# Kernel optimization log

Hardware: AMD Instinct MI355X
Metric: run time of the kernel (lower is better)

Reference implementation:

```python
import jax, jax.numpy as jnp
import numpy as np
from jax import lax

B, A, SEQ, FIN = 512, 16, 50, 6
H, H2, T, G, S = 256, 128, 60, 64, 6
GR0, GR1 = -50.0, 50.0
CELL = (GR1 - GR0) / G
NTYPES, EMB = 10, 16
NENC, NL = 5, 2

def setup_inputs() -> dict:
    key = jax.random.key(0)
    ks = jax.random.split(key, 40)
    def rn(k, shape, scale=0.05):
        return (jax.random.normal(k, shape) * scale).astype(jnp.float32)
    history = jax.random.normal(ks[0], (B, A, SEQ, FIN), dtype=jnp.float32)
    types = jax.random.randint(ks[1], (B,), 0, NTYPES)
    history = history.at[:, 0, 0, 5].set(types.astype(jnp.float32))
    d = dict(history=history)
    d['emb'] = rn(ks[2], (NTYPES, EMB))
    d['fe_W1'] = rn(ks[3], (FIN + EMB, H)); d['fe_b1'] = jnp.zeros((H,), jnp.float32)
    d['fe_W2'] = rn(ks[4], (H, H));        d['fe_b2'] = jnp.zeros((H,), jnp.float32)
    d['enc_Wih'] = rn(ks[5], (NENC, NL, H, 3 * H))
    d['enc_Whh'] = rn(ks[6], (NENC, NL, H, 3 * H))
    d['enc_bih'] = rn(ks[7], (NENC, NL, 3 * H))
    d['enc_bhh'] = rn(ks[8], (NENC, NL, 3 * H))
    d['dec_Wih0'] = rn(ks[9], (2, 3 * H)); d['dec_Whh0'] = rn(ks[10], (H, 3 * H))
    d['dec_bih0'] = rn(ks[11], (3 * H));   d['dec_bhh0'] = rn(ks[12], (3 * H))
    d['dec_Wih1'] = rn(ks[13], (H, 3 * H)); d['dec_Whh1'] = rn(ks[14], (H, 3 * H))
    d['dec_bih1'] = rn(ks[15], (3 * H));    d['dec_bhh1'] = rn(ks[16], (3 * H))
    d['hg_W1'] = rn(ks[17], (H, H));   d['hg_b1'] = jnp.zeros((H,), jnp.float32)
    d['hg_W2'] = rn(ks[18], (H, H2));  d['hg_b2'] = jnp.zeros((H2,), jnp.float32)
    d['hg_W3'] = rn(ks[19], (H2, T * 2)); d['hg_b3'] = jnp.zeros((T * 2,), jnp.float32)
    d['ce_W1'] = rn(ks[20], (H, H2));  d['ce_b1'] = jnp.zeros((H2,), jnp.float32)
    d['ce_W2'] = rn(ks[21], (H2, T));  d['ce_b2'] = jnp.zeros((T,), jnp.float32)
    d['hp_W1'] = rn(ks[22], (H, H));   d['hp_b1'] = jnp.zeros((H,), jnp.float32)
    d['hp_W2'] = rn(ks[23], (H, G * G)); d['hp_b2'] = jnp.zeros((G * G,), jnp.float32)
    return d

def _gru_cell(xt, h, Wih, Whh, bih, bhh):
    # torch GRU gate order: r, z, n
    gi = xt @ Wih + bih
    gh = h @ Whh + bhh
    Hd = h.shape[-1]
    r = jax.nn.sigmoid(gi[:, :Hd] + gh[:, :Hd])
    z = jax.nn.sigmoid(gi[:, Hd:2 * Hd] + gh[:, Hd:2 * Hd])
    n = jnp.tanh(gi[:, 2 * Hd:] + r * gh[:, 2 * Hd:])
    return (1.0 - z) * n + z * h

def _forward(history, emb, fe_W1, fe_b1, fe_W2, fe_b2,
             enc_Wih, enc_Whh, enc_bih, enc_bhh,
             dec_Wih0, dec_Whh0, dec_bih0, dec_bhh0,
             dec_Wih1, dec_Whh1, dec_bih1, dec_bhh1,
             hg_W1, hg_b1, hg_W2, hg_b2, hg_W3, hg_b3,
             ce_W1, ce_b1, ce_W2, ce_b2, hp_W1, hp_b1, hp_W2, hp_b2):
    ego = history[:, 0]                                   # [B,SEQ,6]
    etype = jnp.clip(ego[:, 0, 5].astype(jnp.int32), 0, 9)
    # type -> encoder index (vehicle,pedestrian,cyclist,bus,default)
    eidx = jnp.array([0, 1, 4, 2, 3, 4, 4, 4, 4, 4], jnp.int32)[etype]
    te = emb[etype]                                       # [B,16]
    x_in = jnp.concatenate([ego, jnp.broadcast_to(te[:, None, :], (B, SEQ, EMB))], axis=-1)
    feat = jax.nn.relu(x_in @ fe_W1 + fe_b1) @ fe_W2 + fe_b2  # [B,SEQ,H]

    # 2-layer GRU with per-example (type-gathered) weights
    x_cur = feat.transpose(1, 0, 2)                       # [SEQ,B,H]
    h_finals = []
    for l in range(NL):
        Wih = enc_Wih[eidx, l]; Whh = enc_Whh[eidx, l]    # [B,H,3H]
        bih = enc_bih[eidx, l]; bhh = enc_bhh[eidx, l]    # [B,3H]
        def step(h, xt, Wih=Wih, Whh=Whh, bih=bih, bhh=bhh):
            gi = jnp.einsum('bd,bdg->bg', xt, Wih) + bih
            gh = jnp.einsum('bh,bhg->bg', h, Whh) + bhh
            r = jax.nn.sigmoid(gi[:, :H] + gh[:, :H])
            z = jax.nn.sigmoid(gi[:, H:2 * H] + gh[:, H:2 * H])
            n = jnp.tanh(gi[:, 2 * H:] + r * gh[:, 2 * H:])
            hn = (1.0 - z) * n + z * h
            return hn, hn
        h_last, ys = lax.scan(step, jnp.zeros((B, H), feat.dtype), x_cur)
        x_cur = ys
        h_finals.append(h_last)
    enc_h0, enc_h1 = h_finals

    # decoder GRU, single timestep: x = last ego position
    x0 = ego[:, -1, :2]
    h0 = _gru_cell(x0, enc_h0, dec_Wih0, dec_Whh0, dec_bih0, dec_bhh0)
    h1 = _gru_cell(h0, enc_h1, dec_Wih1, dec_Whh1, dec_bih1, dec_bhh1)
    last_hidden = h1                                      # [B,H]

    traj = (jax.nn.relu(jax.nn.relu(last_hidden @ hg_W1 + hg_b1) @ hg_W2 + hg_b2) @ hg_W3 + hg_b3)
    traj = traj.reshape(B, T, 2)
    conf = jax.nn.relu(last_hidden @ ce_W1 + ce_b1) @ ce_W2 + ce_b2   # [B,T]

    key = jax.random.key(42)
    k_noise, k_samp = jax.random.split(key)
    noise = jax.random.normal(k_noise, (T, B, H), last_hidden.dtype)
    scale = (0.1 * jnp.arange(T, dtype=last_hidden.dtype) / T)[:, None, None]
    th = last_hidden[None] + noise * scale                # [T,B,H]
    logits = jax.nn.relu(th @ hp_W1 + hp_b1) @ hp_W2 + hp_b2  # [T,B,G*G]

    # vectorized multinomial over (samples, timesteps, batch)
    idx = jax.random.categorical(k_samp, logits, shape=(S - 1, T, B))  # int [S-1,T,B]
    x_idx = (idx % G).astype(jnp.float32)
    y_idx = (idx // G).astype(jnp.float32)
    pts = jnp.stack([GR0 + x_idx * CELL + CELL / 2,
                     GR0 + y_idx * CELL + CELL / 2], axis=-1)  # [S-1,T,B,2]
    pts = pts.transpose(2, 0, 1, 3)                       # [B,S-1,T,2]

    predictions = jnp.concatenate([traj[:, None], pts], axis=1)  # [B,S,T,2]
    decay = jnp.float32(0.9) ** jnp.arange(S, dtype=jnp.float32)
    confidences = conf.mean(axis=1)[:, None] * decay[None, :]    # [B,S]
    return predictions, confidences

def reference(history, emb, fe_W1, fe_b1, fe_W2, fe_b2,
              enc_Wih, enc_Whh, enc_bih, enc_bhh,
              dec_Wih0, dec_Whh0, dec_bih0, dec_bhh0,
              dec_Wih1, dec_Whh1, dec_bih1, dec_bhh1,
              hg_W1, hg_b1, hg_W2, hg_b2, hg_W3, hg_b3,
              ce_W1, ce_b1, ce_W2, ce_b2, hp_W1, hp_b1, hp_W2, hp_b2):
    return _forward(history, emb, fe_W1, fe_b1, fe_W2, fe_b2,
                    enc_Wih, enc_Whh, enc_bih, enc_bhh,
                    dec_Wih0, dec_Whh0, dec_bih0, dec_bhh0,
                    dec_Wih1, dec_Whh1, dec_bih1, dec_bhh1,
                    hg_W1, hg_b1, hg_W2, hg_b2, hg_W3, hg_b3,
                    ce_W1, ce_b1, ce_W2, ce_b2, hp_W1, hp_b1, hp_W2, hp_b2)
```

## Files before the change

kernel.cpp:

```cpp
#include <hip/hip_runtime.h>
#include <stdint.h>
#include <math.h>

#define JAX_PARTITIONABLE 1

#define B_ 512
#define SEQ_ 50
#define H_ 256
#define H2_ 128
#define T_ 60
#define S_ 6
#define EMB_ 16
#define NL_ 2
#define TG_ 768
#define CAT_ 4096
#define GUMBEL_N 629145600u
#define NOISE_N 7864320u

typedef float f32x2 __attribute__((ext_vector_type(2)));

#define PKFMA_LO(acc, w, h) \
  asm("v_pk_fma_f32 %0, %1, %2, %0 op_sel:[0,0,0] op_sel_hi:[1,0,1]" : "+v"(acc) : "v"(w), "v"(h))
#define PKFMA_HI(acc, w, h) \
  asm("v_pk_fma_f32 %0, %1, %2, %0 op_sel:[0,1,0] op_sel_hi:[1,1,1]" : "+v"(acc) : "v"(w), "v"(h))

__host__ __device__ inline uint32_t rotl32(uint32_t x, int r) {
#if defined(__HIP_DEVICE_COMPILE__)
  return __builtin_amdgcn_alignbit(x, x, 32 - r);
#else
  return (x << r) | (x >> (32 - r));
#endif
}

__host__ __device__ inline void tf2x32(uint32_t k0, uint32_t k1, uint32_t x0, uint32_t x1,
                                       uint32_t& o0, uint32_t& o1) {
  uint32_t ks2 = k0 ^ k1 ^ 0x1BD11BDAu;
  x0 += k0; x1 += k1;
#define TFR(r) do { x0 += x1; x1 = rotl32(x1, r); x1 ^= x0; } while (0)
  TFR(13); TFR(15); TFR(26); TFR(6);
  x0 += k1; x1 += ks2 + 1u;
  TFR(17); TFR(29); TFR(16); TFR(24);
  x0 += ks2; x1 += k0 + 2u;
  TFR(13); TFR(15); TFR(26); TFR(6);
  x0 += k0; x1 += k1 + 3u;
  TFR(17); TFR(29); TFR(16); TFR(24);
  x0 += k1; x1 += ks2 + 4u;
  TFR(13); TFR(15); TFR(26); TFR(6);
  x0 += ks2; x1 += k0 + 5u;
#undef TFR
  o0 = x0; o1 = x1;
}

__device__ inline uint32_t jax_bits(uint32_t k0, uint32_t k1, uint32_t i, uint32_t n) {
#if JAX_PARTITIONABLE
  (void)n;
  uint32_t a, b;
  tf2x32(k0, k1, 0u, i, a, b);
  return a ^ b;
#else
  uint32_t half = n >> 1;
  uint32_t lo = (i < half) ? i : (i - half);
  uint32_t a, b;
  tf2x32(k0, k1, lo, lo + half, a, b);
  return (i < half) ? a : b;
#endif
}

__device__ inline float bits_to_f01(uint32_t bits) {
  return __uint_as_float((bits >> 9) | 0x3f800000u) - 1.0f;
}

__device__ inline float erfinv_f(float x) {
  double xd = (double)x;
  float w = (float)(-log((1.0 - xd) * (1.0 + xd)));
  float p;
  if (w < 5.0f) {
    w = __fadd_rn(w, -2.5f);
    p = 2.81022636e-08f;
    p = __fadd_rn(3.43273939e-07f, __fmul_rn(p, w));
    p = __fadd_rn(-3.5233877e-06f, __fmul_rn(p, w));
    p = __fadd_rn(-4.39150654e-06f, __fmul_rn(p, w));
    p = __fadd_rn(0.00021858087f, __fmul_rn(p, w));
    p = __fadd_rn(-0.00125372503f, __fmul_rn(p, w));
    p = __fadd_rn(-0.00417768164f, __fmul_rn(p, w));
    p = __fadd_rn(0.246640727f, __fmul_rn(p, w));
    p = __fadd_rn(1.50140941f, __fmul_rn(p, w));
  } else {
    w = __fadd_rn(__fsqrt_rn(w), -3.0f);
    p = -0.000200214257f;
    p = __fadd_rn(0.000100950558f, __fmul_rn(p, w));
    p = __fadd_rn(0.00134934322f, __fmul_rn(p, w));
    p = __fadd_rn(-0.00367342844f, __fmul_rn(p, w));
    p = __fadd_rn(0.00573950773f, __fmul_rn(p, w));
    p = __fadd_rn(-0.0076224613f, __fmul_rn(p, w));
    p = __fadd_rn(0.00943887047f, __fmul_rn(p, w));
    p = __fadd_rn(1.00167406f, __fmul_rn(p, w));
    p = __fadd_rn(2.83297682f, __fmul_rn(p, w));
  }
  return __fmul_rn(p, x);
}

__device__ inline float gumbel_f32(uint32_t bits) {
  float f = bits_to_f01(bits);
  float u = fmaxf(f, 1.17549435e-38f);
  float l1 = logf(u);
  return -logf(-l1);
}

__device__ inline uint32_t orderkey(float s) {
  uint32_t sb = __float_as_uint(s);
  return (sb & 0x80000000u) ? ~sb : (sb | 0x80000000u);
}

__global__ __launch_bounds__(512) void k_init(const float* __restrict__ hist,
                                              float* __restrict__ x0buf, int* __restrict__ ip) {
  int b = threadIdx.x;
  if (b < B_) {
    float tv = hist[b * 4800 + 5];
    int et = (int)tv;
    et = et < 0 ? 0 : (et > 9 ? 9 : et);
    const int mp[10] = {0, 1, 4, 2, 3, 4, 4, 4, 4, 4};
    ip[b] = et;
    ip[512 + b] = mp[et];
    x0buf[b * 2 + 0] = hist[b * 4800 + 49 * 6 + 0];
    x0buf[b * 2 + 1] = hist[b * 4800 + 49 * 6 + 1];
  }
  __syncthreads();
  if (b == 0) {
    int cnt[5] = {0, 0, 0, 0, 0};
    for (int i = 0; i < B_; i++) cnt[ip[512 + i]]++;
    int off[6];
    off[0] = 0;
    for (int e = 0; e < 5; e++) off[e + 1] = off[e] + cnt[e];
    int pos[5];
    for (int e = 0; e < 5; e++) pos[e] = off[e];
    for (int i = 0; i < B_; i++) { int e = ip[512 + i]; ip[1024 + pos[e]++] = i; }
    int* tbl = ip + 1536;
    int nrt = 0;
    for (int e = 0; e < 5; e++) {
      int n = cnt[e];
      for (int s = 0; s < n; s += 16) {
        tbl[1 + nrt] = e;
        tbl[37 + nrt] = off[e] + s;
        tbl[73 + nrt] = (n - s) < 16 ? (n - s) : 16;
        nrt++;
      }
    }
    tbl[0] = nrt;
  }
}

__global__ void k_zero(uint32_t* p, int n) {
  int i = blockIdx.x * blockDim.x + threadIdx.x;
  if (i < n) p[i] = 0u;
}

__global__ __launch_bounds__(256) void k_pack(const float* __restrict__ Wih,
                                              const float* __restrict__ Whh,
                                              float4* __restrict__ wp) {
  int i = blockIdx.x * 256 + threadIdx.x;
  if (i >= 20 * 65536) return;
  int cl = i & 31;
  int k  = (i >> 5) & 255;
  int cg = (i >> 13) & 7;
  int em = i >> 16;
  int m = em & 1;
  int el = em >> 1;
  int c = cg * 32 + cl;
  const float* W = (m ? Whh : Wih) + (size_t)el * H_ * TG_;
  float4 v;
  v.x = W[k * TG_ + c];
  v.y = W[k * TG_ + H_ + c];
  v.z = W[k * TG_ + 2 * H_ + c];
  v.w = 0.0f;
  wp[i] = v;
}

__global__ __launch_bounds__(256) void k_feat(const float* __restrict__ hist, const float* __restrict__ emb,
    const float* __restrict__ W1, const float* __restrict__ b1,
    const float* __restrict__ W2, const float* __restrict__ b2,
    const int* __restrict__ ip, float* __restrict__ featbuf) {
  __shared__ float xs[16][22];
  __shared__ float t1[16][H_];
  int row0 = blockIdx.x * 16;
  int tid = threadIdx.x;
  for (int idx = tid; idx < 16 * 22; idx += 256) {
    int r = idx / 22, c = idx % 22;
    int g = row0 + r;
    int b = g / SEQ_, s = g % SEQ_;
    xs[r][c] = (c < 6) ? hist[b * 4800 + s * 6 + c] : emb[ip[b] * EMB_ + (c - 6)];
  }
  __syncthreads();
  int j = tid;
  {
    double acc[16];
    for (int r = 0; r < 16; r++) acc[r] = 0.0;
    for (int k = 0; k < 22; k++) {
      double w = (double)W1[k * H_ + j];
      for (int r = 0; r < 16; r++) acc[r] += (double)xs[r][k] * w;
    }
    double bb = (double)b1[j];
    for (int r = 0; r < 16; r++) t1[r][j] = fmaxf((float)(acc[r] + bb), 0.0f);
  }
  __syncthreads();
  {
    double acc[16];
    for (int r = 0; r < 16; r++) acc[r] = 0.0;
    for (int k = 0; k < H_; k++) {
      double w = (double)W2[k * H_ + j];
      for (int r = 0; r < 16; r++) acc[r] += (double)t1[r][k] * w;
    }
    double bb = (double)b2[j];
    for (int r = 0; r < 16; r++) {
      float v = (float)(acc[r] + bb);
      int g = row0 + r;
      int b = g / SEQ_, s = g % SEQ_;
      featbuf[(size_t)s * (B_ * H_) + (size_t)b * H_ + j] = v;
    }
  }
}

__device__ __forceinline__ void gi_block_p(float (*xs)[H_], int* rowb,
    int rt, int cg, int tid,
    const float* __restrict__ x, float* __restrict__ gi_out,
    const float4* __restrict__ wpack, const float* __restrict__ bih_base,
    int layer, const int* __restrict__ ip) {
  const int* tbl = ip + 1536;
  const int* order = ip + 1024;
  int nrt = tbl[0];
  if (rt >= nrt) return;
  int e = tbl[1 + rt];
  int start = tbl[37 + rt];
  int nr = tbl[73 + rt];
  for (int idx = tid; idx < 16 * H_; idx += 256) {
    int r = idx >> 8, k = idx & 255;
    int rr = (r < nr) ? r : 0;
    int b = order[start + rr];
    if (k == 0) rowb[r] = b;
    xs[r][k] = x[b * H_ + k];
  }
  __syncthreads();
  int j = tid & 31, rs = tid >> 5;
  int c = cg * 32 + j;
  int el = e * NL_ + layer;
  const float4* wp = wpack + (((size_t)(el * 2 + 0) * 8 + cg) * 256) * 32 + j;
  const float* bih = bih_base + (size_t)el * TG_;
  double ar0 = 0, ar1 = 0, az0 = 0, az1 = 0, an0 = 0, an1 = 0;
  for (int k = 0; k < H_; k += 4) {
    float4 w0 = wp[(k + 0) * 32], w1 = wp[(k + 1) * 32];
    float4 w2 = wp[(k + 2) * 32], w3 = wp[(k + 3) * 32];
    float4 xa = *(const float4*)&xs[rs][k];
    float4 xb = *(const float4*)&xs[rs + 8][k];
    ar0 += (double)xa.x * (double)w0.x; ar1 += (double)xb.x * (double)w0.x;
    az0 += (double)xa.x * (double)w0.y; az1 += (double)xb.x * (double)w0.y;
    an0 += (double)xa.x * (double)w0.z; an1 += (double)xb.x * (double)w0.z;
    ar0 += (double)xa.y * (double)w1.x; ar1 += (double)xb.y * (double)w1.x;
    az0 += (double)xa.y * (double)w1.y; az1 += (double)xb.y * (double)w1.y;
    an0 += (double)xa.y * (double)w1.z; an1 += (double)xb.y * (double)w1.z;
    ar0 += (double)xa.z * (double)w2.x; ar1 += (double)xb.z * (double)w2.x;
    az0 += (double)xa.z * (double)w2.y; az1 += (double)xb.z * (double)w2.y;
    an0 += (double)xa.z * (double)w2.z; an1 += (double)xb.z * (double)w2.z;
    ar0 += (double)xa.w * (double)w3.x; ar1 += (double)xb.w * (double)w3.x;
    az0 += (double)xa.w * (double)w3.y; az1 += (double)xb.w * (double)w3.y;
    an0 += (double)xa.w * (double)w3.z; an1 += (double)xb.w * (double)w3.z;
  }
  int cr = c, cz = H_ + c, cn = 2 * H_ + c;
  double br = (double)bih[cr], bz = (double)bih[cz], bn = (double)bih[cn];
  for (int p = 0; p < 2; p++) {
    int r = rs + 8 * p;
    if (r >= nr) continue;
    int b = rowb[r];
    gi_out[b * TG_ + cr] = (float)((p ? ar1 : ar0) + br);
    gi_out[b * TG_ + cz] = (float)((p ? az1 : az0) + bz);
    gi_out[b * TG_ + cn] = (float)((p ? an1 : an0) + bn);
  }
}

__device__ __forceinline__ void step_block_p(float (*hs)[H_], int* rowb,
    int rt, int cg, int tid,
    const float* __restrict__ gi_in, const float* __restrict__ hin,
    float* __restrict__ hout, float* __restrict__ ys,
    const float4* __restrict__ wpack, const float* __restrict__ bhh_base,
    int layer, const int* __restrict__ ip) {
  const int* tbl = ip + 1536;
  const int* order = ip + 1024;
  int nrt = tbl[0];
  if (rt >= nrt) return;
  int e = tbl[1 + rt];
  int start = tbl[37 + rt];
  int nr = tbl[73 + rt];
  for (int idx = tid; idx < 16 * H_; idx += 256) {
    int r = idx >> 8, k = idx & 255;
    int rr = (r < nr) ? r : 0;
    int b = order[start + rr];
    if (k == 0) rowb[r] = b;
    hs[r][k] = hin[b * H_ + k];
  }
  __syncthreads();
  int j = tid & 31, rs = tid >> 5;
  int c = cg * 32 + j;
  int el = e * NL_ + layer;
  const float4* wp = wpack + (((size_t)(el * 2 + 1) * 8 + cg) * 256) * 32 + j;
  const float* bhh = bhh_base + (size_t)el * TG_;
  double gr0 = 0, gr1 = 0, gz0 = 0, gz1 = 0, gn0 = 0, gn1 = 0;
  for (int k = 0; k < H_; k += 4) {
    float4 w0 = wp[(k + 0) * 32], w1 = wp[(k + 1) * 32];
    float4 w2 = wp[(k + 2) * 32], w3 = wp[(k + 3) * 32];
    float4 ha = *(const float4*)&hs[rs][k];
    float4 hb = *(const float4*)&hs[rs + 8][k];
    gr0 += (double)ha.x * (double)w0.x; gr1 += (double)hb.x * (double)w0.x;
    gz0 += (double)ha.x * (double)w0.y; gz1 += (double)hb.x * (double)w0.y;
    gn0 += (double)ha.x * (double)w0.z; gn1 += (double)hb.x * (double)w0.z;
    gr0 += (double)ha.y * (double)w1.x; gr1 += (double)hb.y * (double)w1.x;
    gz0 += (double)ha.y * (double)w1.y; gz1 += (double)hb.y * (double)w1.y;
    gn0 += (double)ha.y * (double)w1.z; gn1 += (double)hb.y * (double)w1.z;
    gr0 += (double)ha.z * (double)w2.x; gr1 += (double)hb.z * (double)w2.x;
    gz0 += (double)ha.z * (double)w2.y; gz1 += (double)hb.z * (double)w2.y;
    gn0 += (double)ha.z * (double)w2.z; gn1 += (double)hb.z * (double)w2.z;
    gr0 += (double)ha.w * (double)w3.x; gr1 += (double)hb.w * (double)w3.x;
    gz0 += (double)ha.w * (double)w3.y; gz1 += (double)hb.w * (double)w3.y;
    gn0 += (double)ha.w * (double)w3.z; gn1 += (double)hb.w * (double)w3.z;
  }
  int cr = c, cz = H_ + c, cn = 2 * H_ + c;
  double bhr = (double)bhh[cr], bhz = (double)bhh[cz], bhn = (double)bhh[cn];
  for (int p = 0; p < 2; p++) {
    int r = rs + 8 * p;
    if (r >= nr) continue;
    int b = rowb[r];
    double gir = (double)gi_in[b * TG_ + cr];
    double giz = (double)gi_in[b * TG_ + cz];
    double gin = (double)gi_in[b * TG_ + cn];
    double ghr = (p ? gr1 : gr0) + bhr;
    double ghz = (p ? gz1 : gz0) + bhz;
    double ghn = (p ? gn1 : gn0) + bhn;
    double rr = 1.0 / (1.0 + exp(-(gir + ghr)));
    double zz = 1.0 / (1.0 + exp(-(giz + ghz)));
    double nn = tanh(gin + rr * ghn);
    double hv = (double)hs[r][c];
    float hnew = (float)((1.0 - zz) * nn + zz * hv);
    hout[b * H_ + c] = hnew;
    if (ys) ys[b * H_ + c] = hnew;
  }
}

__device__ __forceinline__ void gi_block_u(float (*xs)[H_], int* rowb,
    int rt, int cg, int tid,
    const float* __restrict__ x, float* __restrict__ gi_out,
    const float* __restrict__ Wih_base, const float* __restrict__ bih_base,
    int layer, const int* __restrict__ ip) {
  const int* tbl = ip + 1536;
  const int* order = ip + 1024;
  int nrt = tbl[0];
  if (rt >= nrt) return;
  int e = tbl[1 + rt];
  int start = tbl[37 + rt];
  int nr = tbl[73 + rt];
  for (int idx = tid; idx < 16 * H_; idx += 256) {
    int r = idx >> 8, k = idx & 255;
    int rr = (r < nr) ? r : 0;
    int b = order[start + rr];
    if (k == 0) rowb[r] = b;
    xs[r][k] = x[b * H_ + k];
  }
  __syncthreads();
  size_t woff = (size_t)(e * NL_ + layer);
  const float* Wih = Wih_base + woff * (size_t)H_ * TG_;
  const float* bih = bih_base + woff * TG_;
  int j = tid & 31, rs = tid >> 5;
  int c = cg * 32 + j;
  int cr = c, cz = H_ + c, cn = 2 * H_ + c;
  double ar0 = 0, ar1 = 0, az0 = 0, az1 = 0, an0 = 0, an1 = 0;
  for (int k = 0; k < H_; k++) {
    float wr = Wih[k * TG_ + cr], wz = Wih[k * TG_ + cz], wn = Wih[k * TG_ + cn];
    float x0 = xs[rs][k], x1 = xs[rs + 8][k];
    ar0 += (double)x0 * wr; ar1 += (double)x1 * wr;
    az0 += (double)x0 * wz; az1 += (double)x1 * wz;
    an0 += (double)x0 * wn; an1 += (double)x1 * wn;
  }
  double br = (double)bih[cr], bz = (double)bih[cz], bn = (double)bih[cn];
  for (int p = 0; p < 2; p++) {
    int r = rs + 8 * p;
    if (r >= nr) continue;
    int b = rowb[r];
    gi_out[b * TG_ + cr] = (float)((p ? ar1 : ar0) + br);
    gi_out[b * TG_ + cz] = (float)((p ? az1 : az0) + bz);
    gi_out[b * TG_ + cn] = (float)((p ? an1 : an0) + bn);
  }
}

__device__ __forceinline__ void step_block_u(float (*hs)[H_], int* rowb,
    int rt, int cg, int tid,
    const float* __restrict__ gi_in, const float* __restrict__ hin,
    float* __restrict__ hout, float* __restrict__ ys,
    const float* __restrict__ Whh_base, const float* __restrict__ bhh_base,
    int layer, const int* __restrict__ ip) {
  const int* tbl = ip + 1536;
  const int* order = ip + 1024;
  int nrt = tbl[0];
  if (rt >= nrt) return;
  int e = tbl[1 + rt];
  int start = tbl[37 + rt];
  int nr = tbl[73 + rt];
  for (int idx = tid; idx < 16 * H_; idx += 256) {
    int r = idx >> 8, k = idx & 255;
    int rr = (r < nr) ? r : 0;
    int b = order[start + rr];
    if (k == 0) rowb[r] = b;
    hs[r][k] = hin[b * H_ + k];
  }
  __syncthreads();
  size_t woff = (size_t)(e * NL_ + layer);
  const float* Whh = Whh_base + woff * (size_t)H_ * TG_;
  const float* bhh = bhh_base + woff * TG_;
  int j = tid & 31, rs = tid >> 5;
  int c = cg * 32 + j;
  int cr = c, cz = H_ + c, cn = 2 * H_ + c;
  double gr0 = 0, gr1 = 0, gz0 = 0, gz1 = 0, gn0 = 0, gn1 = 0;
  for (int k = 0; k < H_; k++) {
    float wr = Whh[k * TG_ + cr], wz = Whh[k * TG_ + cz], wn = Whh[k * TG_ + cn];
    float h0 = hs[rs][k], h1 = hs[rs + 8][k];
    gr0 += (double)h0 * wr; gr1 += (double)h1 * wr;
    gz0 += (double)h0 * wz; gz1 += (double)h1 * wz;
    gn0 += (double)h0 * wn; gn1 += (double)h1 * wn;
  }
  double bhr = (double)bhh[cr], bhz = (double)bhh[cz], bhn = (double)bhh[cn];
  for (int p = 0; p < 2; p++) {
    int r = rs + 8 * p;
    if (r >= nr) continue;
    int b = rowb[r];
    double gir = (double)gi_in[b * TG_ + cr];
    double giz = (double)gi_in[b * TG_ + cz];
    double gin = (double)gi_in[b * TG_ + cn];
    double ghr = (p ? gr1 : gr0) + bhr;
    double ghz = (p ? gz1 : gz0) + bhz;
    double ghn = (p ? gn1 : gn0) + bhn;
    double rr = 1.0 / (1.0 + exp(-(gir + ghr)));
    double zz = 1.0 / (1.0 + exp(-(giz + ghz)));
    double nn = tanh(gin + rr * ghn);
    double hv = (double)hs[r][c];
    float hnew = (float)((1.0 - zz) * nn + zz * hv);
    hout[b * H_ + c] = hnew;
    if (ys) ys[b * H_ + c] = hnew;
  }
}

template <bool PACKED>
__global__ __launch_bounds__(256) void k_pipe(int d,
    const float* __restrict__ feat, float* __restrict__ ys0,
    float* __restrict__ gi0, float* __restrict__ gi1,
    float* __restrict__ h0A, float* __restrict__ h0B,
    float* __restrict__ h1A, float* __restrict__ h1B,
    const float* __restrict__ Wih, const float* __restrict__ Whh,
    const float* __restrict__ bih, const float* __restrict__ bhh,
    const float4* __restrict__ wpack, const int* __restrict__ ip) {
  __shared__ float sb[16][H_];
  __shared__ int rowb[16];
  int g = blockIdx.x;
  int grp = g / 288, bx = g % 288;
  int rt = bx >> 3, cg = bx & 7;
  int tid = threadIdx.x;
  if (grp == 0) {
    int t = d; if (t >= SEQ_) return;
    if (PACKED) gi_block_p(sb, rowb, rt, cg, tid, feat + (size_t)t * 131072,
                           gi0 + (size_t)(t & 1) * 393216, wpack, bih, 0, ip);
    else        gi_block_u(sb, rowb, rt, cg, tid, feat + (size_t)t * 131072,
                           gi0 + (size_t)(t & 1) * 393216, Wih, bih, 0, ip);
  } else if (grp == 1) {
    int t = d - 1; if (t < 0 || t >= SEQ_) return;
    const float* hin = (t & 1) ? h0B : h0A;
    float* hout = (t & 1) ? h0A : h0B;
    if (PACKED) step_block_p(sb, rowb, rt, cg, tid, gi0 + (size_t)(t & 1) * 393216,
                             hin, hout, ys0 + (size_t)t * 131072, wpack, bhh, 0, ip);
    else        step_block_u(sb, rowb, rt, cg, tid, gi0 + (size_t)(t & 1) * 393216,
                             hin, hout, ys0 + (size_t)t * 131072, Whh, bhh, 0, ip);
  } else if (grp == 2) {
    int t = d - 2; if (t < 0 || t >= SEQ_) return;
    if (PACKED) gi_block_p(sb, rowb, rt, cg, tid, ys0 + (size_t)t * 131072,
                           gi1 + (size_t)(t & 1) * 393216, wpack, bih, 1, ip);
    else        gi_block_u(sb, rowb, rt, cg, tid, ys0 + (size_t)t * 131072,
                           gi1 + (size_t)(t & 1) * 393216, Wih, bih, 1, ip);
  } else {
    int t = d - 3; if (t < 0 || t >= SEQ_) return;
    const float* hin = (t & 1) ? h1B : h1A;
    float* hout = (t & 1) ? h1A : h1B;
    if (PACKED) step_block_p(sb, rowb, rt, cg, tid, gi1 + (size_t)(t & 1) * 393216,
                             hin, hout, nullptr, wpack, bhh, 1, ip);
    else        step_block_u(sb, rowb, rt, cg, tid, gi1 + (size_t)(t & 1) * 393216,
                             hin, hout, nullptr, Whh, bhh, 1, ip);
  }
}

template <int D1>
__global__ __launch_bounds__(256) void k_gru(
    const float* __restrict__ x, const float* __restrict__ hin,
    float* __restrict__ hout,
    const float* __restrict__ Wih, const float* __restrict__ Whh,
    const float* __restrict__ bih, const float* __restrict__ bhh) {
  __shared__ float xs[16][(D1 == 2) ? 2 : H_];
  __shared__ float hs[16][H_];
  int bx = blockIdx.x, by = blockIdx.y;
  int start = bx * 16;
  int tid = threadIdx.x;
  for (int idx = tid; idx < 16 * H_; idx += 256) {
    int r = idx >> 8, k = idx & 255;
    int b = start + r;
    hs[r][k] = hin[b * H_ + k];
    if (D1 == H_) xs[r][k] = x[b * H_ + k];
    else if (k < D1) xs[r][k] = x[b * D1 + k];
  }
  __syncthreads();
  int j = tid & 31, rs = tid >> 5;
  int hc = by * 32 + j;
  int cr = hc, cz = H_ + hc, cn = 2 * H_ + hc;
  double ra0 = 0, ra1 = 0, za0 = 0, za1 = 0, ni0 = 0, ni1 = 0, nh0 = 0, nh1 = 0;
  for (int k = 0; k < H_; k++) {
    float wrh = Whh[k * TG_ + cr], wzh = Whh[k * TG_ + cz], wnh = Whh[k * TG_ + cn];
    float h0v = hs[rs][k], h1v = hs[rs + 8][k];
    ra0 += (double)h0v * wrh; ra1 += (double)h1v * wrh;
    za0 += (double)h0v * wzh; za1 += (double)h1v * wzh;
    nh0 += (double)h0v * wnh; nh1 += (double)h1v * wnh;
    if (D1 == H_) {
      float wri = Wih[k * TG_ + cr], wzi = Wih[k * TG_ + cz], wni = Wih[k * TG_ + cn];
      float x0v = xs[rs][k], x1v = xs[rs + 8][k];
      ra0 += (double)x0v * wri; ra1 += (double)x1v * wri;
      za0 += (double)x0v * wzi; za1 += (double)x1v * wzi;
      ni0 += (double)x0v * wni; ni1 += (double)x1v * wni;
    }
  }
  if (D1 != H_) {
    for (int k = 0; k < D1; k++) {
      float wri = Wih[k * TG_ + cr], wzi = Wih[k * TG_ + cz], wni = Wih[k * TG_ + cn];
      float x0v = xs[rs][k], x1v = xs[rs + 8][k];
      ra0 += (double)x0v * wri; ra1 += (double)x1v * wri;
      za0 += (double)x0v * wzi; za1 += (double)x1v * wzi;
      ni0 += (double)x0v * wni; ni1 += (double)x1v * wni;
    }
  }
  double br_i = (double)bih[cr], bz_i = (double)bih[cz], bn_i = (double)bih[cn];
  double br_h = (double)bhh[cr], bz_h = (double)bhh[cz], bn_h = (double)bhh[cn];
  for (int p = 0; p < 2; p++) {
    int r = rs + 8 * p;
    double ra = p ? ra1 : ra0, za = p ? za1 : za0, ni = p ? ni1 : ni0, nh = p ? nh1 : nh0;
    double rr = 1.0 / (1.0 + exp(-(ra + br_i + br_h)));
    double zz = 1.0 / (1.0 + exp(-(za + bz_i + bz_h)));
    double nn = tanh((ni + bn_i) + rr * (nh + bn_h));
    double hv = (double)hs[r][hc];
    float hnew = (float)((1.0 - zz) * nn + zz * hv);
    hout[(start + r) * H_ + hc] = hnew;
  }
}

__global__ __launch_bounds__(256) void k_heads(const float* __restrict__ lh,
    const float* __restrict__ hgW1, const float* __restrict__ hgb1,
    const float* __restrict__ hgW2, const float* __restrict__ hgb2,
    const float* __restrict__ hgW3, const float* __restrict__ hgb3,
    const float* __restrict__ ceW1, const float* __restrict__ ceb1,
    const float* __restrict__ ceW2, const float* __restrict__ ceb2,
    float* __restrict__ out) {
  __shared__ float hsm[16][H_];
  __shared__ float t1[16][H_];
  __shared__ float t2[16][H2_];
  __shared__ float c2s[16][T_];
  int row0 = blockIdx.x * 16;
  int tid = threadIdx.x;
  for (int idx = tid; idx < 16 * H_; idx += 256) {
    int r = idx >> 8, k = idx & 255;
    hsm[r][k] = lh[(size_t)(row0 + r) * H_ + k];
  }
  __syncthreads();
  {
    int j = tid;
    for (int r = 0; r < 16; r++) {
      double a = 0;
      for (int k = 0; k < H_; k++) a += (double)hsm[r][k] * (double)hgW1[k * H_ + j];
      t1[r][j] = fmaxf((float)(a + (double)hgb1[j]), 0.0f);
    }
  }
  __syncthreads();
  if (tid < H2_) {
    int j = tid;
    for (int r = 0; r < 16; r++) {
      double a = 0;
      for (int k = 0; k < H_; k++) a += (double)t1[r][k] * (double)hgW2[k * H2_ + j];
      t2[r][j] = fmaxf((float)(a + (double)hgb2[j]), 0.0f);
    }
  }
  __syncthreads();
  if (tid < 2 * T_) {
    int j = tid;
    for (int r = 0; r < 16; r++) {
      double a = 0;
      for (int k = 0; k < H2_; k++) a += (double)t2[r][k] * (double)hgW3[k * (2 * T_) + j];
      float v = (float)(a + (double)hgb3[j]);
      int b = row0 + r;
      int t = j >> 1, c = j & 1;
      out[(((size_t)b * S_ + 0) * T_ + t) * 2 + c] = v;
    }
  }
  __syncthreads();
  if (tid < H2_) {
    int j = tid;
    for (int r = 0; r < 16; r++) {
      double a = 0;
      for (int k = 0; k < H_; k++) a += (double)hsm[r][k] * (double)ceW1[k * H2_ + j];
      t2[r][j] = fmaxf((float)(a + (double)ceb1[j]), 0.0f);
    }
  }
  __syncthreads();
  if (tid < T_) {
    int j = tid;
    for (int r = 0; r < 16; r++) {
      double a = 0;
      for (int k = 0; k < H2_; k++) a += (double)t2[r][k] * (double)ceW2[k * T_ + j];
      c2s[r][j] = (float)(a + (double)ceb2[j]);
    }
  }
  __syncthreads();
  if (tid < 16) {
    int r = tid;
    int b = row0 + r;
    double s = 0;
    for (int j = 0; j < T_; j++) s += (double)c2s[r][j];
    float m = (float)(s / 60.0);
    for (int sd = 0; sd < S_; sd++) {
      float d = (float)pow((double)0.9f, (double)sd);
      out[368640 + b * S_ + sd] = __fmul_rn(m, d);
    }
  }
}

__global__ __launch_bounds__(256) void k_hp1(const float* __restrict__ lh,
    const float* __restrict__ W1, const float* __restrict__ b1,
    float* __restrict__ h1buf, uint32_t nk0, uint32_t nk1) {
  __shared__ float th[16][H_];
  int row0 = blockIdx.x * 16;
  int tid = threadIdx.x;
  const float SQRT2F = 1.4142135623730951f;
  const float LO = -0x1.fffffep-1f;
  for (int idx = tid; idx < 16 * H_; idx += 256) {
    int r = idx >> 8, k = idx & 255;
    int g = row0 + r;
    int t = g / B_, b = g % B_;
    uint32_t i = ((uint32_t)t * B_ + (uint32_t)b) * H_ + (uint32_t)k;
    uint32_t bits = jax_bits(nk0, nk1, i, NOISE_N);
    float f = bits_to_f01(bits);
    float u = fmaxf(LO, __fadd_rn(__fmul_rn(f, 2.0f), LO));
    float nz = __fmul_rn(SQRT2F, erfinv_f(u));
    float sc = __fdiv_rn(__fmul_rn(0.1f, (float)t), 60.0f);
    th[r][k] = __fadd_rn(lh[(size_t)b * H_ + k], __fmul_rn(nz, sc));
  }
  __syncthreads();
  int j = tid;
  double acc[16];
  for (int r = 0; r < 16; r++) acc[r] = 0.0;
  for (int k = 0; k < H_; k++) {
    double w = (double)W1[k * H_ + j];
    for (int r = 0; r < 16; r++) acc[r] += (double)th[r][k] * w;
  }
  double bb = (double)b1[j];
  for (int r = 0; r < 16; r++)
    h1buf[(size_t)(row0 + r) * H_ + j] = fmaxf((float)(acc[r] + bb), 0.0f);
}

__global__ __launch_bounds__(256) void k_hp2(const float* __restrict__ h1buf,
    const float* __restrict__ W2, const float* __restrict__ b2,
    unsigned long long* __restrict__ samples, uint32_t sk0, uint32_t sk1) {
  __shared__ float h1[16][H_];
  int row0 = blockIdx.x * 16;
  int cat0 = blockIdx.y * 256;
  int tid = threadIdx.x;
  for (int idx = tid; idx < 16 * H_ / 4; idx += 256) {
    int r = idx >> 6, k4 = (idx & 63) << 2;
    *(float4*)&h1[r][k4] = *(const float4*)&h1buf[(size_t)(row0 + r) * H_ + k4];
  }
  __syncthreads();
  int wave = tid >> 6;
  int lane = tid & 63;
  int catA = cat0 + 4 * lane;
  int rbase = 4 * wave;

  f32x2 acc[4][2];
#pragma unroll
  for (int r = 0; r < 4; r++) { acc[r][0] = (f32x2)0.0f; acc[r][1] = (f32x2)0.0f; }
  const float* w2p = W2 + catA;
  for (int k = 0; k < H_; k += 4) {
    float4 hv[4];
    hv[0] = *(const float4*)&h1[rbase + 0][k];
    hv[1] = *(const float4*)&h1[rbase + 1][k];
    hv[2] = *(const float4*)&h1[rbase + 2][k];
    hv[3] = *(const float4*)&h1[rbase + 3][k];
    float4 wv[4];
#pragma unroll
    for (int kk = 0; kk < 4; kk++) wv[kk] = *(const float4*)&w2p[(size_t)(k + kk) * CAT_];
#pragma unroll
    for (int kk = 0; kk < 4; kk++) {
      f32x2 wlo; wlo.x = wv[kk].x; wlo.y = wv[kk].y;
      f32x2 whi; whi.x = wv[kk].z; whi.y = wv[kk].w;
#pragma unroll
      for (int r = 0; r < 4; r++) {
        f32x2 hp;
        if (kk & 2) { hp.x = (&hv[r].x)[2]; hp.y = (&hv[r].x)[3]; }
        else        { hp.x = (&hv[r].x)[0]; hp.y = (&hv[r].x)[1]; }
        if (kk & 1) { PKFMA_HI(acc[r][0], wlo, hp); PKFMA_HI(acc[r][1], whi, hp); }
        else        { PKFMA_LO(acc[r][0], wlo, hp); PKFMA_LO(acc[r][1], whi, hp); }
      }
    }
  }
  float lg[4][4];
  float4 b4 = *(const float4*)&b2[catA];
#pragma unroll
  for (int r = 0; r < 4; r++) {
    lg[r][0] = __fadd_rn(acc[r][0].x, b4.x);
    lg[r][1] = __fadd_rn(acc[r][0].y, b4.y);
    lg[r][2] = __fadd_rn(acc[r][1].x, b4.z);
    lg[r][3] = __fadd_rn(acc[r][1].y, b4.w);
  }

  int t = row0 / B_;
  int bbase = row0 % B_;
#pragma unroll
  for (int s = 0; s < S_ - 1; s++) {
#pragma unroll
    for (int q = 0; q < 4; q++) {
      int brow = bbase + rbase + q;
      uint32_t ibase = (((uint32_t)s * T_ + (uint32_t)t) * B_ + (uint32_t)brow) * CAT_ + (uint32_t)catA;
      float sc0 = __fadd_rn(gumbel_f32(jax_bits(sk0, sk1, ibase + 0u, GUMBEL_N)), lg[q][0]);
      float sc1 = __fadd_rn(gumbel_f32(jax_bits(sk0, sk1, ibase + 1u, GUMBEL_N)), lg[q][1]);
      float sc2 = __fadd_rn(gumbel_f32(jax_bits(sk0, sk1, ibase + 2u, GUMBEL_N)), lg[q][2]);
      float sc3 = __fadd_rn(gumbel_f32(jax_bits(sk0, sk1, ibase + 3u, GUMBEL_N)), lg[q][3]);
      float bs = sc0; int bc = catA;
      if (sc1 > bs) { bs = sc1; bc = catA + 1; }
      if (sc2 > bs) { bs = sc2; bc = catA + 2; }
      if (sc3 > bs) { bs = sc3; bc = catA + 3; }
      float mv = bs;
      for (int off = 1; off < 64; off <<= 1)
        mv = fmaxf(mv, __shfl_xor(mv, off, 64));
      unsigned long long mask = __ballot(bs == mv);
      int src = __ffsll(mask) - 1;
      int wcat = __shfl(bc, src, 64);
      if (lane == 0) {
        unsigned long long p =
            (((unsigned long long)orderkey(mv)) << 32) | (unsigned long long)(~(uint32_t)wcat);
        atomicMax(&samples[((size_t)s * T_ + t) * B_ + brow], p);
      }
    }
  }
}

__global__ void k_emit(const unsigned long long* __restrict__ samples, float* __restrict__ out) {
  int gid = blockIdx.x * blockDim.x + threadIdx.x;
  if (gid >= (S_ - 1) * T_ * B_) return;
  int b = gid % B_;
  int t = (gid / B_) % T_;
  int s = gid / (B_ * T_);
  unsigned long long v = samples[gid];
  uint32_t cat = ~(uint32_t)(v & 0xFFFFFFFFu);
  float xi = (float)(cat & 63u);
  float yi = (float)(cat >> 6);
  float px = -50.0f + xi * 1.5625f + 0.78125f;
  float py = -50.0f + yi * 1.5625f + 0.78125f;
  size_t o = (((size_t)b * S_ + (size_t)(s + 1)) * T_ + t) * 2;
  out[o] = px;
  out[o + 1] = py;
}

extern "C" void kernel_launch(void* const* d_in, const int* in_sizes, int n_in,
                              void* d_out, int out_size, void* d_ws, size_t ws_size,
                              hipStream_t stream) {
  (void)in_sizes; (void)n_in; (void)out_size;
  const float* hist   = (const float*)d_in[0];
  const float* emb    = (const float*)d_in[1];
  const float* feW1   = (const float*)d_in[2];
  const float* feb1   = (const float*)d_in[3];
  const float* feW2   = (const float*)d_in[4];
  const float* feb2   = (const float*)d_in[5];
  const float* encWih = (const float*)d_in[6];
  const float* encWhh = (const float*)d_in[7];
  const float* encbih = (const float*)d_in[8];
  const float* encbhh = (const float*)d_in[9];
  const float* dWih0  = (const float*)d_in[10];
  const float* dWhh0  = (const float*)d_in[11];
  const float* dbih0  = (const float*)d_in[12];
  const float* dbhh0  = (const float*)d_in[13];
  const float* dWih1  = (const float*)d_in[14];
  const float* dWhh1  = (const float*)d_in[15];
  const float* dbih1  = (const float*)d_in[16];
  const float* dbhh1  = (const float*)d_in[17];
  const float* hgW1   = (const float*)d_in[18];
  const float* hgb1   = (const float*)d_in[19];
  const float* hgW2   = (const float*)d_in[20];
  const float* hgb2   = (const float*)d_in[21];
  const float* hgW3   = (const float*)d_in[22];
  const float* hgb3   = (const float*)d_in[23];
  const float* ceW1   = (const float*)d_in[24];
  const float* ceb1   = (const float*)d_in[25];
  const float* ceW2   = (const float*)d_in[26];
  const float* ceb2   = (const float*)d_in[27];
  const float* hpW1   = (const float*)d_in[28];
  const float* hpb1   = (const float*)d_in[29];
  const float* hpW2   = (const float*)d_in[30];
  const float* hpb2   = (const float*)d_in[31];
  float* out = (float*)d_out;
  float* ws = (float*)d_ws;

  float* feat  = ws;
  float* ys0   = ws + 6553600;
  float* gi0   = ws + 13107200;
  float* gi1   = ws + 13893632;
  float* h0A   = ws + 14680064;
  float* h0B   = h0A + 131072;
  float* h1A   = h0B + 131072;
  float* h1B   = h1A + 131072;
  float* dech0 = h1B + 131072;
  float* lh    = dech0 + 131072;
  float* x0buf = lh + 131072;
  int*   ip    = (int*)(x0buf + 1024);
  unsigned long long* samples =
      (unsigned long long*)(((uintptr_t)(ip + 2048) + 255) & ~(uintptr_t)255);
  float* h1hp  = ws;

  size_t samples_end = (size_t)((char*)(samples + 307200) - (char*)ws);
  size_t wpack_off = (samples_end + 255) & ~(size_t)255;
  float4* wpack = (float4*)((char*)ws + wpack_off);
  bool packed = (wpack_off + (size_t)20 * 65536 * 16) <= ws_size;

  uint32_t kn0, kn1, ks0, ks1;
#if JAX_PARTITIONABLE
  tf2x32(0u, 42u, 0u, 0u, kn0, kn1);
  tf2x32(0u, 42u, 0u, 1u, ks0, ks1);
#else
  { uint32_t a0, a1, b0, b1;
    tf2x32(0u, 42u, 0u, 2u, a0, a1);
    tf2x32(0u, 42u, 1u, 3u, b0, b1);
    kn0 = a0; kn1 = b0; ks0 = a1; ks1 = b1; }
#endif

  k_init<<<dim3(1), dim3(512), 0, stream>>>(hist, x0buf, ip);
  k_zero<<<dim3((524288 + 255) / 256), dim3(256), 0, stream>>>((uint32_t*)h0A, 524288);
  k_zero<<<dim3((307200 + 255) / 256), dim3(256), 0, stream>>>((uint32_t*)samples, 307200);
  if (packed)
    k_pack<<<dim3(5120), dim3(256), 0, stream>>>(encWih, encWhh, wpack);
  k_feat<<<dim3(1600), dim3(256), 0, stream>>>(hist, emb, feW1, feb1, feW2, feb2, ip, feat);

  for (int d = 0; d < SEQ_ + 3; d++) {
    if (packed)
      k_pipe<true><<<dim3(1152), dim3(256), 0, stream>>>(d,
          feat, ys0, gi0, gi1, h0A, h0B, h1A, h1B,
          encWih, encWhh, encbih, encbhh, wpack, ip);
    else
      k_pipe<false><<<dim3(1152), dim3(256), 0, stream>>>(d,
          feat, ys0, gi0, gi1, h0A, h0B, h1A, h1B,
          encWih, encWhh, encbih, encbhh, wpack, ip);
  }

  k_gru<2><<<dim3(32, 8), dim3(256), 0, stream>>>(
      x0buf, h0A, dech0, dWih0, dWhh0, dbih0, dbhh0);
  k_gru<H_><<<dim3(32, 8), dim3(256), 0, stream>>>(
      dech0, h1A, lh, dWih1, dWhh1, dbih1, dbhh1);

  k_heads<<<dim3(32), dim3(256), 0, stream>>>(lh, hgW1, hgb1, hgW2, hgb2, hgW3, hgb3,
                                              ceW1, ceb1, ceW2, ceb2, out);
  k_hp1<<<dim3(1920), dim3(256), 0, stream>>>(lh, hpW1, hpb1, h1hp, kn0, kn1);
  k_hp2<<<dim3(1920, 16), dim3(256), 0, stream>>>(h1hp, hpW2, hpb2, samples, ks0, ks1);
  k_emit<<<dim3(600), dim3(256), 0, stream>>>(samples, out);
}
```

Measured before the change: 5.600 ms.

## Fuse encoder pipeline launches into one persistent kernel with grid barrier

Replaces the 53 per-step launches of the encoder pipeline kernel with a single persistent kernel that loops over the diagonal steps and synchronises all blocks through an atomic-counter grid barrier. The aim is to remove per-launch overhead and the idle gaps between dependent steps. The persistent path is taken only when occupancy queries show all 1152 blocks can be resident at once; otherwise it falls back to per-step launches. The barrier adds atomic spinning and fence costs, and the counter is cleared by extending the existing zeroing launch.

Measured after the change: 5.601 ms. About the same (+0.0%).

```diff
diff --git a/kernel.cpp b/kernel.cpp
--- a/kernel.cpp
+++ b/kernel.cpp
@@ -16,6 +16,7 @@
 #define CAT_ 4096
 #define GUMBEL_N 629145600u
 #define NOISE_N 7864320u
+#define ENC_BLOCKS 1152
 
 typedef float f32x2 __attribute__((ext_vector_type(2)));
 
@@ -112,6 +113,18 @@
   return (sb & 0x80000000u) ? ~sb : (sb | 0x80000000u);
 }
 
+__device__ __forceinline__ void gbar(unsigned int* bar, unsigned int target) {
+  __syncthreads();
+  if (threadIdx.x == 0) {
+    __threadfence();
+    __hip_atomic_fetch_add(bar, 1u, __ATOMIC_RELEASE, __HIP_MEMORY_SCOPE_AGENT);
+    while (__hip_atomic_load(bar, __ATOMIC_ACQUIRE, __HIP_MEMORY_SCOPE_AGENT) < target)
+      __builtin_amdgcn_s_sleep(8);
+    __threadfence();
+  }
+  __syncthreads();
+}
+
 __global__ __launch_bounds__(512) void k_init(const float* __restrict__ hist,
                                               float* __restrict__ x0buf, int* __restrict__ ip) {
   int b = threadIdx.x;
@@ -343,6 +356,79 @@
   }
 }
 
+__device__ __forceinline__ void pipe_body(int d, int grp, int rt, int cg, int tid,
+    float (*sb)[H_], int* rowb,
+    const float* feat, float* ys0, float* gi0, float* gi1,
+    float* h0A, float* h0B, float* h1A, float* h1B,
+    const float4* wpack, const float* bih, const float* bhh, const int* ip) {
+  if (grp == 0) {
+    int t = d;
+    if (t < SEQ_)
+      gi_block_p(sb, rowb, rt, cg, tid, feat + (size_t)t * 131072,
+                 gi0 + (size_t)(t & 1) * 393216, wpack, bih, 0, ip);
+  } else if (grp == 1) {
+    int t = d - 1;
+    if (t >= 0 && t < SEQ_) {
+      const float* hin = (t & 1) ? h0B : h0A;
+      float* hout = (t & 1) ? h0A : h0B;
+      step_block_p(sb, rowb, rt, cg, tid, gi0 + (size_t)(t & 1) * 393216,
+                   hin, hout, ys0 + (size_t)t * 131072, wpack, bhh, 0, ip);
+    }
+  } else if (grp == 2) {
+    int t = d - 2;
+    if (t >= 0 && t < SEQ_)
+      gi_block_p(sb, rowb, rt, cg, tid, ys0 + (size_t)t * 131072,
+                 gi1 + (size_t)(t & 1) * 393216, wpack, bih, 1, ip);
+  } else {
+    int t = d - 3;
+    if (t >= 0 && t < SEQ_) {
+      const float* hin = (t & 1) ? h1B : h1A;
+      float* hout = (t & 1) ? h1A : h1B;
+      step_block_p(sb, rowb, rt, cg, tid, gi1 + (size_t)(t & 1) * 393216,
+                   hin, hout, nullptr, wpack, bhh, 1, ip);
+    }
+  }
+}
+
+__global__ __launch_bounds__(256, 8) void k_enc(
+    const float* __restrict__ feat, float* __restrict__ ys0,
+    float* __restrict__ gi0, float* __restrict__ gi1,
+    float* __restrict__ h0A, float* __restrict__ h0B,
+    float* __restrict__ h1A, float* __restrict__ h1B,
+    const float4* __restrict__ wpack,
+    const float* __restrict__ bih, const float* __restrict__ bhh,
+    const int* __restrict__ ip, unsigned int* __restrict__ bar) {
+  __shared__ float sb[16][H_];
+  __shared__ int rowb[16];
+  int g = blockIdx.x;
+  int grp = g / 288, bx = g % 288;
+  int rt = bx >> 3, cg = bx & 7;
+  int tid = threadIdx.x;
+  for (int d = 0; d < SEQ_ + 3; d++) {
+    if (d) gbar(bar, (unsigned)(ENC_BLOCKS * d));
+    pipe_body(d, grp, rt, cg, tid, sb, rowb, feat, ys0, gi0, gi1,
+              h0A, h0B, h1A, h1B, wpack, bih, bhh, ip);
+  }
+}
+
+__global__ __launch_bounds__(256) void k_pipep(int d,
+    const float* __restrict__ feat, float* __restrict__ ys0,
+    float* __restrict__ gi0, float* __restrict__ gi1,
+    float* __restrict__ h0A, float* __restrict__ h0B,
+    float* __restrict__ h1A, float* __restrict__ h1B,
+    const float4* __restrict__ wpack,
+    const float* __restrict__ bih, const float* __restrict__ bhh,
+    const int* __restrict__ ip) {
+  __shared__ float sb[16][H_];
+  __shared__ int rowb[16];
+  int g = blockIdx.x;
+  int grp = g / 288, bx = g % 288;
+  int rt = bx >> 3, cg = bx & 7;
+  int tid = threadIdx.x;
+  pipe_body(d, grp, rt, cg, tid, sb, rowb, feat, ys0, gi0, gi1,
+            h0A, h0B, h1A, h1B, wpack, bih, bhh, ip);
+}
+
 __device__ __forceinline__ void gi_block_u(float (*xs)[H_], int* rowb,
     int rt, int cg, int tid,
     const float* __restrict__ x, float* __restrict__ gi_out,
@@ -444,15 +530,14 @@
   }
 }
 
-template <bool PACKED>
-__global__ __launch_bounds__(256) void k_pipe(int d,
+__global__ __launch_bounds__(256) void k_pipeu(int d,
     const float* __restrict__ feat, float* __restrict__ ys0,
     float* __restrict__ gi0, float* __restrict__ gi1,
     float* __restrict__ h0A, float* __restrict__ h0B,
     float* __restrict__ h1A, float* __restrict__ h1B,
     const float* __restrict__ Wih, const float* __restrict__ Whh,
     const float* __restrict__ bih, const float* __restrict__ bhh,
-    const float4* __restrict__ wpack, const int* __restrict__ ip) {
+    const int* __restrict__ ip) {
   __shared__ float sb[16][H_];
   __shared__ int rowb[16];
   int g = blockIdx.x;
@@ -461,32 +546,24 @@
   int tid = threadIdx.x;
   if (grp == 0) {
     int t = d; if (t >= SEQ_) return;
-    if (PACKED) gi_block_p(sb, rowb, rt, cg, tid, feat + (size_t)t * 131072,
-                           gi0 + (size_t)(t & 1) * 393216, wpack, bih, 0, ip);
-    else        gi_block_u(sb, rowb, rt, cg, tid, feat + (size_t)t * 131072,
-                           gi0 + (size_t)(t & 1) * 393216, Wih, bih, 0, ip);
+    gi_block_u(sb, rowb, rt, cg, tid, feat + (size_t)t * 131072,
+               gi0 + (size_t)(t & 1) * 393216, Wih, bih, 0, ip);
   } else if (grp == 1) {
     int t = d - 1; if (t < 0 || t >= SEQ_) return;
     const float* hin = (t & 1) ? h0B : h0A;
     float* hout = (t & 1) ? h0A : h0B;
-    if (PACKED) step_block_p(sb, rowb, rt, cg, tid, gi0 + (size_t)(t & 1) * 393216,
-                             hin, hout, ys0 + (size_t)t * 131072, wpack, bhh, 0, ip);
-    else        step_block_u(sb, rowb, rt, cg, tid, gi0 + (size_t)(t & 1) * 393216,
-                             hin, hout, ys0 + (size_t)t * 131072, Whh, bhh, 0, ip);
+    step_block_u(sb, rowb, rt, cg, tid, gi0 + (size_t)(t & 1) * 393216,
+                 hin, hout, ys0 + (size_t)t * 131072, Whh, bhh, 0, ip);
   } else if (grp == 2) {
     int t = d - 2; if (t < 0 || t >= SEQ_) return;
-    if (PACKED) gi_block_p(sb, rowb, rt, cg, tid, ys0 + (size_t)t * 131072,
-                           gi1 + (size_t)(t & 1) * 393216, wpack, bih, 1, ip);
-    else        gi_block_u(sb, rowb, rt, cg, tid, ys0 + (size_t)t * 131072,
-                           gi1 + (size_t)(t & 1) * 393216, Wih, bih, 1, ip);
+    gi_block_u(sb, rowb, rt, cg, tid, ys0 + (size_t)t * 131072,
+               gi1 + (size_t)(t & 1) * 393216, Wih, bih, 1, ip);
   } else {
     int t = d - 3; if (t < 0 || t >= SEQ_) return;
     const float* hin = (t & 1) ? h1B : h1A;
     float* hout = (t & 1) ? h1A : h1B;
-    if (PACKED) step_block_p(sb, rowb, rt, cg, tid, gi1 + (size_t)(t & 1) * 393216,
-                             hin, hout, nullptr, wpack, bhh, 1, ip);
-    else        step_block_u(sb, rowb, rt, cg, tid, gi1 + (size_t)(t & 1) * 393216,
-                             hin, hout, nullptr, Whh, bhh, 1, ip);
+    step_block_u(sb, rowb, rt, cg, tid, gi1 + (size_t)(t & 1) * 393216,
+                 hin, hout, nullptr, Whh, bhh, 1, ip);
   }
 }
 
@@ -818,11 +895,24 @@
   unsigned long long* samples =
       (unsigned long long*)(((uintptr_t)(ip + 2048) + 255) & ~(uintptr_t)255);
   float* h1hp  = ws;
+  unsigned int* bar = (unsigned int*)((uint32_t*)samples + 307200);
 
   size_t samples_end = (size_t)((char*)(samples + 307200) - (char*)ws);
   size_t wpack_off = (samples_end + 255) & ~(size_t)255;
   float4* wpack = (float4*)((char*)ws + wpack_off);
   bool packed = (wpack_off + (size_t)20 * 65536 * 16) <= ws_size;
+
+  bool persistent = false;
+  if (packed) {
+    int dev = 0;
+    if (hipGetDevice(&dev) == hipSuccess) {
+      int numCU = 0, occ = 0;
+      if (hipDeviceGetAttribute(&numCU, hipDeviceAttributeMultiprocessorCount, dev) == hipSuccess &&
+          hipOccupancyMaxActiveBlocksPerMultiprocessor(&occ, k_enc, 256, 0) == hipSuccess) {
+        persistent = ((long long)occ * numCU >= ENC_BLOCKS);
+      }
+    }
+  }
 
   uint32_t kn0, kn1, ks0, ks1;
 #if JAX_PARTITIONABLE
@@ -837,20 +927,25 @@
 
   k_init<<<dim3(1), dim3(512), 0, stream>>>(hist, x0buf, ip);
   k_zero<<<dim3((524288 + 255) / 256), dim3(256), 0, stream>>>((uint32_t*)h0A, 524288);
-  k_zero<<<dim3((307200 + 255) / 256), dim3(256), 0, stream>>>((uint32_t*)samples, 307200);
+  k_zero<<<dim3((307264 + 255) / 256), dim3(256), 0, stream>>>((uint32_t*)samples, 307264);
   if (packed)
     k_pack<<<dim3(5120), dim3(256), 0, stream>>>(encWih, encWhh, wpack);
   k_feat<<<dim3(1600), dim3(256), 0, stream>>>(hist, emb, feW1, feb1, feW2, feb2, ip, feat);
 
-  for (int d = 0; d < SEQ_ + 3; d++) {
-    if (packed)
-      k_pipe<true><<<dim3(1152), dim3(256), 0, stream>>>(d,
+  if (packed && persistent) {
+    k_enc<<<dim3(ENC_BLOCKS), dim3(256), 0, stream>>>(
+        feat, ys0, gi0, gi1, h0A, h0B, h1A, h1B,
+        wpack, encbih, encbhh, ip, bar);
+  } else if (packed) {
+    for (int d = 0; d < SEQ_ + 3; d++)
+      k_pipep<<<dim3(ENC_BLOCKS), dim3(256), 0, stream>>>(d,
           feat, ys0, gi0, gi1, h0A, h0B, h1A, h1B,
-          encWih, encWhh, encbih, encbhh, wpack, ip);
-    else
-      k_pipe<false><<<dim3(1152), dim3(256), 0, stream>>>(d,
+          wpack, encbih, encbhh, ip);
+  } else {
+    for (int d = 0; d < SEQ_ + 3; d++)
+      k_pipeu<<<dim3(ENC_BLOCKS), dim3(256), 0, stream>>>(d,
           feat, ys0, gi0, gi1, h0A, h0B, h1A, h1B,
-          encWih, encWhh, encbih, encbhh, wpack, ip);
+          encWih, encWhh, encbih, encbhh, ip);
   }
 
   k_gru<2><<<dim3(32, 8), dim3(256), 0, stream>>>(
```
